# Kernel tuning notes

Measured on AMD Instinct MI355X. Metric: run time of the kernel, lower is better.

The kernel has to match this reference:

```python
import jax, jax.numpy as jnp
import numpy as np

N = 100000
SAMPLE = 25
FEAT = 128
HIDDEN = 128
CLASSES = 40


def setup_inputs() -> dict:
    key = jax.random.key(0)
    k_x, k_n, k_w1, k_w2, k_wl = jax.random.split(key, 5)
    X = jax.random.normal(k_x, (N, FEAT), dtype=jnp.float32)
    neighbors = jax.random.randint(k_n, (N, SAMPLE), 0, N, dtype=jnp.int32)
    # torch Linear weights are [out_features, in_features], xavier-uniform init
    def xavier(k, out_d, in_d):
        bound = float(np.sqrt(6.0 / (in_d + out_d)))
        return jax.random.uniform(k, (out_d, in_d), dtype=jnp.float32, minval=-bound, maxval=bound)
    W1 = xavier(k_w1, HIDDEN, FEAT)
    W2 = xavier(k_w2, HIDDEN, HIDDEN)
    Wlast = xavier(k_wl, CLASSES, HIDDEN)
    return {"X": X, "neighbors": neighbors, "W1": W1, "W2": W2, "Wlast": Wlast}


def reference(X, neighbors, W1, W2, Wlast):
    # forward: for each layer W: X = spmm(adj, X); X = X @ W.T; relu(X)
    # adj row i has sample_num entries of value 1/sample_num -> mean over sampled neighbors
    h = X
    for W in (W1, W2):
        agg = jnp.mean(h[neighbors], axis=1)          # [N, sample, d] -> [N, d]
        h = jax.nn.relu(jnp.einsum('nd,hd->nh', agg, W))
    return jnp.einsum('nh,ch->nc', h, Wlast)          # [N, class_num]
```

## Files before the change

kernel.cpp:

```cpp
#include <hip/hip_runtime.h>
#include <cstdint>
#include <cstddef>

typedef unsigned short u16;
typedef __bf16 bf16x8 __attribute__((ext_vector_type(8)));
typedef u16 u16x8 __attribute__((ext_vector_type(8)));
typedef float f32x4 __attribute__((ext_vector_type(4)));

#define N_NODES 100000
#define SAMPLE 25
#define FEAT 128
#define CLASSES 40

__device__ __forceinline__ float bf2f(u16 v) {
    return __uint_as_float(((unsigned)v) << 16);
}
__device__ __forceinline__ u16 f2bf(float f) {
    unsigned u = __float_as_uint(f);
    u += 0x7FFFu + ((u >> 16) & 1u);
    return (u16)(u >> 16);
}
__device__ __forceinline__ void split_bf(float x, u16& hi, u16& lo) {
    hi = f2bf(x);
    lo = f2bf(x - bf2f(hi));
}

__device__ __forceinline__ void split8(const float* ap, bf16x8& ah, bf16x8& al) {
    union { u16x8 u; bf16x8 b; } H, L;
    #pragma unroll
    for (int j = 0; j < 8; ++j) {
        u16 h, lo; split_bf(ap[j], h, lo);
        H.u[j] = h; L.u[j] = lo;
    }
    ah = H.b; al = L.b;
}

__device__ __forceinline__ f32x4 mfma_split(bf16x8 ah, bf16x8 al,
                                            bf16x8 bh, bf16x8 bl, f32x4 acc) {
    acc = __builtin_amdgcn_mfma_f32_16x16x32_bf16(ah, bh, acc, 0, 0, 0);
    acc = __builtin_amdgcn_mfma_f32_16x16x32_bf16(al, bh, acc, 0, 0, 0);
    acc = __builtin_amdgcn_mfma_f32_16x16x32_bf16(ah, bl, acc, 0, 0, 0);
    return acc;
}

__global__ __launch_bounds__(256) void prep_weights(
    const float* __restrict__ W1, const float* __restrict__ W2,
    const float* __restrict__ Wl,
    u16* __restrict__ w1h, u16* __restrict__ w1l,
    u16* __restrict__ w2h, u16* __restrict__ w2l,
    u16* __restrict__ wlh, u16* __restrict__ wll)
{
    const int i = blockIdx.x * 256 + threadIdx.x;
    const int stride = gridDim.x * 256;
    for (int j = i; j < FEAT * FEAT; j += stride) {
        split_bf(W1[j], w1h[j], w1l[j]);
        split_bf(W2[j], w2h[j], w2l[j]);
    }
    for (int j = i; j < CLASSES * FEAT; j += stride) {
        split_bf(Wl[j], wlh[j], wll[j]);
    }
}

#define NPB32 32
#define ZT_STRIDE 136

__global__ __launch_bounds__(128, 4) void k1_gemm(
    const float* __restrict__ X,
    const u16* __restrict__ w1h, const u16* __restrict__ w1l,
    u16* __restrict__ Z1)
{
    __shared__ u16 zt[NPB32][ZT_STRIDE];

    const int t = threadIdx.x;
    const int w  = t >> 6;
    const int l  = t & 63;
    const int lr = l & 15;
    const int lq = l >> 4;
    const int blockStart = blockIdx.x * NPB32;
    const float* Xrow = X + (size_t)(blockStart + w * 16 + lr) * FEAT;

    bf16x8 ah[4], al[4];
    #pragma unroll
    for (int k = 0; k < 4; ++k) {
        f32x4 x0 = *(const f32x4*)(Xrow + k * 32 + lq * 8);
        f32x4 x1 = *(const f32x4*)(Xrow + k * 32 + lq * 8 + 4);
        float tmp[8];
        #pragma unroll
        for (int j = 0; j < 4; ++j) { tmp[j] = x0[j]; tmp[4 + j] = x1[j]; }
        split8(tmp, ah[k], al[k]);
    }

    #pragma unroll
    for (int c = 0; c < 8; ++c) {
        f32x4 acc = {0.f, 0.f, 0.f, 0.f};
        #pragma unroll
        for (int k = 0; k < 4; ++k) {
            const size_t off = (size_t)(c * 16 + lr) * FEAT + k * 32 + lq * 8;
            bf16x8 bh = *(const bf16x8*)(w1h + off);
            bf16x8 bl = *(const bf16x8*)(w1l + off);
            acc = mfma_split(ah[k], al[k], bh, bl, acc);
        }
        #pragma unroll
        for (int r = 0; r < 4; ++r)
            zt[w * 16 + lq * 4 + r][c * 16 + lr] = f2bf(acc[r]);
    }
    __syncthreads();

    #pragma unroll
    for (int p = 0; p < 4; ++p) {
        const int idx = p * 128 + t;
        const int row = idx >> 4;
        const int col = (idx & 15) * 8;
        *(u16x8*)(Z1 + (size_t)(blockStart + row) * FEAT + col) =
            *(const u16x8*)&zt[row][col];
    }
}

__global__ __launch_bounds__(128, 3) void k2_hop(
    const u16* __restrict__ Zin, const int* __restrict__ nb,
    const u16* __restrict__ wh, const u16* __restrict__ wl,
    u16* __restrict__ Zout)
{
    __shared__ int nbs[NPB32 * SAMPLE];
    __shared__ float agg[NPB32][132];

    const int t = threadIdx.x;
    const int blockStart = blockIdx.x * NPB32;

    for (int i = t; i < NPB32 * SAMPLE; i += 128)
        nbs[i] = nb[blockStart * SAMPLE + i];
    __syncthreads();

    #pragma unroll 1
    for (int it = 0; it < 4; ++it) {
        const int item = t + it * 128;
        const int nl = item >> 4;
        const int fg = item & 15;
        const int* myn = &nbs[nl * SAMPLE];
        u16x8 buf[SAMPLE];
        #pragma unroll
        for (int s = 0; s < SAMPLE; ++s)
            buf[s] = *(const u16x8*)(Zin + ((size_t)myn[s] << 7) + fg * 8);
        float acc[8];
        #pragma unroll
        for (int j = 0; j < 8; ++j) acc[j] = 0.f;
        #pragma unroll
        for (int s = 0; s < SAMPLE; ++s) {
            #pragma unroll
            for (int j = 0; j < 8; ++j) acc[j] += bf2f(buf[s][j]);
        }
        #pragma unroll
        for (int j = 0; j < 8; ++j) {
            float m = acc[j] * (1.0f / SAMPLE);
            agg[nl][fg * 8 + j] = m > 0.f ? m : 0.f;
        }
    }
    __syncthreads();

    const int w  = t >> 6;
    const int l  = t & 63;
    const int lr = l & 15;
    const int lq = l >> 4;

    bf16x8 ah[4], al[4];
    #pragma unroll
    for (int k = 0; k < 4; ++k)
        split8(&agg[w * 16 + lr][k * 32 + lq * 8], ah[k], al[k]);
    __syncthreads();

    u16* zt = (u16*)agg;

    #pragma unroll
    for (int c = 0; c < 8; ++c) {
        f32x4 acc = {0.f, 0.f, 0.f, 0.f};
        #pragma unroll
        for (int k = 0; k < 4; ++k) {
            const size_t off = (size_t)(c * 16 + lr) * FEAT + k * 32 + lq * 8;
            bf16x8 bh = *(const bf16x8*)(wh + off);
            bf16x8 bl = *(const bf16x8*)(wl + off);
            acc = mfma_split(ah[k], al[k], bh, bl, acc);
        }
        #pragma unroll
        for (int r = 0; r < 4; ++r)
            zt[(size_t)(w * 16 + lq * 4 + r) * ZT_STRIDE + c * 16 + lr] = f2bf(acc[r]);
    }
    __syncthreads();

    #pragma unroll
    for (int p = 0; p < 4; ++p) {
        const int idx = p * 128 + t;
        const int row = idx >> 4;
        const int col = (idx & 15) * 8;
        *(u16x8*)(Zout + (size_t)(blockStart + row) * FEAT + col) =
            *(const u16x8*)&zt[(size_t)row * ZT_STRIDE + col];
    }
}

__global__ __launch_bounds__(128, 3) void k3_hop(
    const u16* __restrict__ Zin, const int* __restrict__ nb,
    const u16* __restrict__ wh, const u16* __restrict__ wl,
    float* __restrict__ out)
{
    __shared__ int nbs[NPB32 * SAMPLE];
    __shared__ float agg[NPB32][132];

    const int t = threadIdx.x;
    const int blockStart = blockIdx.x * NPB32;

    for (int i = t; i < NPB32 * SAMPLE; i += 128)
        nbs[i] = nb[blockStart * SAMPLE + i];
    __syncthreads();

    #pragma unroll 1
    for (int it = 0; it < 4; ++it) {
        const int item = t + it * 128;
        const int nl = item >> 4;
        const int fg = item & 15;
        const int* myn = &nbs[nl * SAMPLE];
        u16x8 buf[SAMPLE];
        #pragma unroll
        for (int s = 0; s < SAMPLE; ++s)
            buf[s] = *(const u16x8*)(Zin + ((size_t)myn[s] << 7) + fg * 8);
        float acc[8];
        #pragma unroll
        for (int j = 0; j < 8; ++j) acc[j] = 0.f;
        #pragma unroll
        for (int s = 0; s < SAMPLE; ++s) {
            #pragma unroll
            for (int j = 0; j < 8; ++j) acc[j] += bf2f(buf[s][j]);
        }
        #pragma unroll
        for (int j = 0; j < 8; ++j) {
            float m = acc[j] * (1.0f / SAMPLE);
            agg[nl][fg * 8 + j] = m > 0.f ? m : 0.f;
        }
    }
    __syncthreads();

    const int w  = t >> 6;
    const int l  = t & 63;
    const int lr = l & 15;
    const int lq = l >> 4;

    bf16x8 ah[4], al[4];
    #pragma unroll
    for (int k = 0; k < 4; ++k)
        split8(&agg[w * 16 + lr][k * 32 + lq * 8], ah[k], al[k]);

    #pragma unroll
    for (int c = 0; c < 3; ++c) {
        const int o = c * 16 + lr;
        f32x4 acc = {0.f, 0.f, 0.f, 0.f};
        #pragma unroll
        for (int k = 0; k < 4; ++k) {
            bf16x8 bh, bl;
            if (o < CLASSES) {
                const size_t off = (size_t)o * FEAT + k * 32 + lq * 8;
                bh = *(const bf16x8*)(wh + off);
                bl = *(const bf16x8*)(wl + off);
            } else {
                #pragma unroll
                for (int j = 0; j < 8; ++j) { bh[j] = (__bf16)0.f; bl[j] = (__bf16)0.f; }
            }
            acc = mfma_split(ah[k], al[k], bh, bl, acc);
        }
        if (o < CLASSES) {
            #pragma unroll
            for (int r = 0; r < 4; ++r) {
                const int node = blockStart + w * 16 + lq * 4 + r;
                out[(size_t)node * CLASSES + o] = acc[r];
            }
        }
    }
}

#define NPB 64
#define AGG_STRIDE 136

__global__ __launch_bounds__(256) void gnn_layer1(
    const float* __restrict__ X, const int* __restrict__ nb,
    const u16* __restrict__ w1h, const u16* __restrict__ w1l,
    u16* __restrict__ h1)
{
    __shared__ int nbs[NPB * SAMPLE];
    __shared__ u16 agg_h[NPB][AGG_STRIDE];
    __shared__ u16 agg_l[NPB][AGG_STRIDE];

    const int t = threadIdx.x;
    const int blockStart = blockIdx.x * NPB;

    for (int i = t; i < NPB * SAMPLE; i += 256) {
        int gi = blockStart * SAMPLE + i;
        if (gi >= N_NODES * SAMPLE) gi = N_NODES * SAMPLE - 1;
        nbs[i] = nb[gi];
    }
    __syncthreads();

    for (int item = t; item < NPB * 16; item += 256) {
        const int nl = item >> 4;
        const int fg = item & 15;
        float acc[8];
        #pragma unroll
        for (int j = 0; j < 8; ++j) acc[j] = 0.f;
        const int* myn = &nbs[nl * SAMPLE];
        for (int s = 0; s < SAMPLE; ++s) {
            const float4* p = (const float4*)(X + (size_t)myn[s] * FEAT + fg * 8);
            float4 a = p[0], b = p[1];
            acc[0] += a.x; acc[1] += a.y; acc[2] += a.z; acc[3] += a.w;
            acc[4] += b.x; acc[5] += b.y; acc[6] += b.z; acc[7] += b.w;
        }
        u16x8 oh, ol;
        #pragma unroll
        for (int j = 0; j < 8; ++j) {
            float m = acc[j] * (1.0f / SAMPLE);
            u16 h, lo; split_bf(m, h, lo);
            oh[j] = h; ol[j] = lo;
        }
        *(u16x8*)&agg_h[nl][fg * 8] = oh;
        *(u16x8*)&agg_l[nl][fg * 8] = ol;
    }
    __syncthreads();

    const int w  = t >> 6;
    const int l  = t & 63;
    const int lr = l & 15;
    const int lq = l >> 4;

    bf16x8 ah[4], al[4];
    #pragma unroll
    for (int k = 0; k < 4; ++k) {
        ah[k] = *(const bf16x8*)&agg_h[w * 16 + lr][k * 32 + lq * 8];
        al[k] = *(const bf16x8*)&agg_l[w * 16 + lr][k * 32 + lq * 8];
    }

    #pragma unroll
    for (int c = 0; c < 8; ++c) {
        f32x4 acc = {0.f, 0.f, 0.f, 0.f};
        #pragma unroll
        for (int k = 0; k < 4; ++k) {
            const size_t off = (size_t)(c * 16 + lr) * FEAT + k * 32 + lq * 8;
            bf16x8 bh = *(const bf16x8*)(w1h + off);
            bf16x8 bl = *(const bf16x8*)(w1l + off);
            acc = mfma_split(ah[k], al[k], bh, bl, acc);
        }
        #pragma unroll
        for (int r = 0; r < 4; ++r) {
            int node = blockStart + w * 16 + lq * 4 + r;
            if (node < N_NODES) {
                float v = acc[r] > 0.f ? acc[r] : 0.f;
                h1[(size_t)node * FEAT + c * 16 + lr] = f2bf(v);
            }
        }
    }
}

__global__ __launch_bounds__(256) void gnn_layer2_final(
    const u16* __restrict__ h1, const int* __restrict__ nb,
    const u16* __restrict__ w2h, const u16* __restrict__ w2l,
    const u16* __restrict__ wlh, const u16* __restrict__ wll,
    float* __restrict__ out)
{
    __shared__ int nbs[NPB * SAMPLE];
    __shared__ u16 agg_h[NPB][AGG_STRIDE];
    __shared__ u16 agg_l[NPB][AGG_STRIDE];

    const int t = threadIdx.x;
    const int blockStart = blockIdx.x * NPB;

    for (int i = t; i < NPB * SAMPLE; i += 256) {
        int gi = blockStart * SAMPLE + i;
        if (gi >= N_NODES * SAMPLE) gi = N_NODES * SAMPLE - 1;
        nbs[i] = nb[gi];
    }
    __syncthreads();

    for (int item = t; item < NPB * 16; item += 256) {
        const int nl = item >> 4;
        const int fg = item & 15;
        float acc[8];
        #pragma unroll
        for (int j = 0; j < 8; ++j) acc[j] = 0.f;
        const int* myn = &nbs[nl * SAMPLE];
        for (int s = 0; s < SAMPLE; ++s) {
            u16x8 v = *(const u16x8*)(h1 + (size_t)myn[s] * FEAT + fg * 8);
            #pragma unroll
            for (int j = 0; j < 8; ++j) acc[j] += bf2f(v[j]);
        }
        u16x8 oh, ol;
        #pragma unroll
        for (int j = 0; j < 8; ++j) {
            float m = acc[j] * (1.0f / SAMPLE);
            u16 h, lo; split_bf(m, h, lo);
            oh[j] = h; ol[j] = lo;
        }
        *(u16x8*)&agg_h[nl][fg * 8] = oh;
        *(u16x8*)&agg_l[nl][fg * 8] = ol;
    }
    __syncthreads();

    const int w  = t >> 6;
    const int l  = t & 63;
    const int lr = l & 15;
    const int lq = l >> 4;

    f32x4 hacc[8];
    {
        bf16x8 ah[4], al[4];
        #pragma unroll
        for (int k = 0; k < 4; ++k) {
            ah[k] = *(const bf16x8*)&agg_h[w * 16 + lr][k * 32 + lq * 8];
            al[k] = *(const bf16x8*)&agg_l[w * 16 + lr][k * 32 + lq * 8];
        }
        #pragma unroll
        for (int c = 0; c < 8; ++c) {
            f32x4 acc = {0.f, 0.f, 0.f, 0.f};
            #pragma unroll
            for (int k = 0; k < 4; ++k) {
                const size_t off = (size_t)(c * 16 + lr) * FEAT + k * 32 + lq * 8;
                bf16x8 bh = *(const bf16x8*)(w2h + off);
                bf16x8 bl = *(const bf16x8*)(w2l + off);
                acc = mfma_split(ah[k], al[k], bh, bl, acc);
            }
            hacc[c] = acc;
        }
    }
    __syncthreads();

    #pragma unroll
    for (int c = 0; c < 8; ++c) {
        #pragma unroll
        for (int r = 0; r < 4; ++r) {
            float v = hacc[c][r] > 0.f ? hacc[c][r] : 0.f;
            u16 h, l2; split_bf(v, h, l2);
            agg_h[w * 16 + lq * 4 + r][c * 16 + lr] = h;
            agg_l[w * 16 + lq * 4 + r][c * 16 + lr] = l2;
        }
    }
    __syncthreads();

    {
        bf16x8 ah[4], al[4];
        #pragma unroll
        for (int k = 0; k < 4; ++k) {
            ah[k] = *(const bf16x8*)&agg_h[w * 16 + lr][k * 32 + lq * 8];
            al[k] = *(const bf16x8*)&agg_l[w * 16 + lr][k * 32 + lq * 8];
        }
        #pragma unroll
        for (int c = 0; c < 3; ++c) {
            const int o = c * 16 + lr;
            f32x4 acc = {0.f, 0.f, 0.f, 0.f};
            #pragma unroll
            for (int k = 0; k < 4; ++k) {
                bf16x8 bh, bl;
                if (o < CLASSES) {
                    const size_t off = (size_t)o * FEAT + k * 32 + lq * 8;
                    bh = *(const bf16x8*)(wlh + off);
                    bl = *(const bf16x8*)(wll + off);
                } else {
                    #pragma unroll
                    for (int j = 0; j < 8; ++j) { bh[j] = (__bf16)0.f; bl[j] = (__bf16)0.f; }
                }
                acc = mfma_split(ah[k], al[k], bh, bl, acc);
            }
            if (o < CLASSES) {
                #pragma unroll
                for (int r = 0; r < 4; ++r) {
                    int node = blockStart + w * 16 + lq * 4 + r;
                    if (node < N_NODES) {
                        out[(size_t)node * CLASSES + o] = acc[r];
                    }
                }
            }
        }
    }
}

extern "C" void kernel_launch(void* const* d_in, const int* in_sizes, int n_in,
                              void* d_out, int out_size, void* d_ws, size_t ws_size,
                              hipStream_t stream) {
    const float* X  = (const float*)d_in[0];
    const int*   nb = (const int*)d_in[1];
    const float* W1 = (const float*)d_in[2];
    const float* W2 = (const float*)d_in[3];
    const float* Wl = (const float*)d_in[4];
    float* out = (float*)d_out;

    const size_t zelems = (size_t)N_NODES * FEAT;
    const size_t welems = 4 * (size_t)FEAT * FEAT + 2 * (size_t)CLASSES * FEAT;
    const size_t need_fast = (2 * zelems + welems) * sizeof(u16);

    if (ws_size >= need_fast) {
        u16* Z1  = (u16*)d_ws;
        u16* Z2  = Z1 + zelems;
        u16* w1h = Z2 + zelems;
        u16* w1l = w1h + FEAT * FEAT;
        u16* w2h = w1l + FEAT * FEAT;
        u16* w2l = w2h + FEAT * FEAT;
        u16* wlh = w2l + FEAT * FEAT;
        u16* wll = wlh + CLASSES * FEAT;

        prep_weights<<<64, 256, 0, stream>>>(W1, W2, Wl, w1h, w1l, w2h, w2l, wlh, wll);
        const int blocks = N_NODES / NPB32;
        k1_gemm<<<blocks, 128, 0, stream>>>(X, w1h, w1l, Z1);
        k2_hop<<<blocks, 128, 0, stream>>>(Z1, nb, w2h, w2l, Z2);
        k3_hop<<<blocks, 128, 0, stream>>>(Z2, nb, wlh, wll, out);
    } else {
        u16* h1  = (u16*)d_ws;
        u16* w1h = h1 + zelems;
        u16* w1l = w1h + FEAT * FEAT;
        u16* w2h = w1l + FEAT * FEAT;
        u16* w2l = w2h + FEAT * FEAT;
        u16* wlh = w2l + FEAT * FEAT;
        u16* wll = wlh + CLASSES * FEAT;

        prep_weights<<<64, 256, 0, stream>>>(W1, W2, Wl, w1h, w1l, w2h, w2l, wlh, wll);
        const int blocks = (N_NODES + NPB - 1) / NPB;
        gnn_layer1<<<blocks, 256, 0, stream>>>(X, nb, w1h, w1l, h1);
        gnn_layer2_final<<<blocks, 256, 0, stream>>>(h1, nb, w2h, w2l, wlh, wll, out);
    }
}
```

Before: 328.6 us.

## Gather neighbor features directly into MFMA fragment layout, dropping LDS staging

The hop kernels now have each lane gather and sum the neighbor feature slices it needs for its MFMA A-fragment. The mean, relu and hi/lo split happen in registers, so the shared-memory float aggregation buffer and one barrier are gone. Less LDS lets the occupancy hint go from 3 to 4 blocks per CU. The risk is that each lane now issues four 16-byte loads per neighbor with a different coalescing pattern, and the accumulators use more registers.

```diff
diff --git a/kernel.cpp b/kernel.cpp
--- a/kernel.cpp
+++ b/kernel.cpp
@@ -116,73 +116,74 @@
     }
 }
 
-__global__ __launch_bounds__(128, 3) void k2_hop(
+__global__ __launch_bounds__(128, 4) void k2_hop(
     const u16* __restrict__ Zin, const int* __restrict__ nb,
     const u16* __restrict__ wh, const u16* __restrict__ wl,
     u16* __restrict__ Zout)
 {
     __shared__ int nbs[NPB32 * SAMPLE];
-    __shared__ float agg[NPB32][132];
+    __shared__ u16 zt[NPB32][ZT_STRIDE];
 
     const int t = threadIdx.x;
     const int blockStart = blockIdx.x * NPB32;
 
     for (int i = t; i < NPB32 * SAMPLE; i += 128)
         nbs[i] = nb[blockStart * SAMPLE + i];
-    __syncthreads();
-
-    #pragma unroll 1
-    for (int it = 0; it < 4; ++it) {
-        const int item = t + it * 128;
-        const int nl = item >> 4;
-        const int fg = item & 15;
-        const int* myn = &nbs[nl * SAMPLE];
-        u16x8 buf[SAMPLE];
-        #pragma unroll
-        for (int s = 0; s < SAMPLE; ++s)
-            buf[s] = *(const u16x8*)(Zin + ((size_t)myn[s] << 7) + fg * 8);
-        float acc[8];
-        #pragma unroll
-        for (int j = 0; j < 8; ++j) acc[j] = 0.f;
-        #pragma unroll
-        for (int s = 0; s < SAMPLE; ++s) {
-            #pragma unroll
-            for (int j = 0; j < 8; ++j) acc[j] += bf2f(buf[s][j]);
-        }
-        #pragma unroll
-        for (int j = 0; j < 8; ++j) {
-            float m = acc[j] * (1.0f / SAMPLE);
-            agg[nl][fg * 8 + j] = m > 0.f ? m : 0.f;
-        }
-    }
     __syncthreads();
 
     const int w  = t >> 6;
     const int l  = t & 63;
     const int lr = l & 15;
     const int lq = l >> 4;
+    const int* myn = &nbs[(w * 16 + lr) * SAMPLE];
+
+    float acc[4][8];
+    #pragma unroll
+    for (int k = 0; k < 4; ++k)
+        #pragma unroll
+        for (int j = 0; j < 8; ++j) acc[k][j] = 0.f;
+
+    #pragma unroll
+    for (int s = 0; s < SAMPLE; ++s) {
+        const u16* row = Zin + ((size_t)myn[s] << 7) + lq * 8;
+        u16x8 v0 = *(const u16x8*)(row);
+        u16x8 v1 = *(const u16x8*)(row + 32);
+        u16x8 v2 = *(const u16x8*)(row + 64);
+        u16x8 v3 = *(const u16x8*)(row + 96);
+        #pragma unroll
+        for (int j = 0; j < 8; ++j) {
+            acc[0][j] += bf2f(v0[j]);
+            acc[1][j] += bf2f(v1[j]);
+            acc[2][j] += bf2f(v2[j]);
+            acc[3][j] += bf2f(v3[j]);
+        }
+    }
 
     bf16x8 ah[4], al[4];
     #pragma unroll
-    for (int k = 0; k < 4; ++k)
-        split8(&agg[w * 16 + lr][k * 32 + lq * 8], ah[k], al[k]);
-    __syncthreads();
-
-    u16* zt = (u16*)agg;
+    for (int k = 0; k < 4; ++k) {
+        float tmp[8];
+        #pragma unroll
+        for (int j = 0; j < 8; ++j) {
+            float m = acc[k][j] * (1.0f / SAMPLE);
+            tmp[j] = m > 0.f ? m : 0.f;
+        }
+        split8(tmp, ah[k], al[k]);
+    }
 
     #pragma unroll
     for (int c = 0; c < 8; ++c) {
-        f32x4 acc = {0.f, 0.f, 0.f, 0.f};
+        f32x4 o = {0.f, 0.f, 0.f, 0.f};
         #pragma unroll
         for (int k = 0; k < 4; ++k) {
             const size_t off = (size_t)(c * 16 + lr) * FEAT + k * 32 + lq * 8;
             bf16x8 bh = *(const bf16x8*)(wh + off);
             bf16x8 bl = *(const bf16x8*)(wl + off);
-            acc = mfma_split(ah[k], al[k], bh, bl, acc);
+            o = mfma_split(ah[k], al[k], bh, bl, o);
         }
         #pragma unroll
         for (int r = 0; r < 4; ++r)
-            zt[(size_t)(w * 16 + lq * 4 + r) * ZT_STRIDE + c * 16 + lr] = f2bf(acc[r]);
+            zt[w * 16 + lq * 4 + r][c * 16 + lr] = f2bf(o[r]);
     }
     __syncthreads();
 
@@ -192,65 +193,68 @@
         const int row = idx >> 4;
         const int col = (idx & 15) * 8;
         *(u16x8*)(Zout + (size_t)(blockStart + row) * FEAT + col) =
-            *(const u16x8*)&zt[(size_t)row * ZT_STRIDE + col];
-    }
-}
-
-__global__ __launch_bounds__(128, 3) void k3_hop(
+            *(const u16x8*)&zt[row][col];
+    }
+}
+
+__global__ __launch_bounds__(128, 4) void k3_hop(
     const u16* __restrict__ Zin, const int* __restrict__ nb,
     const u16* __restrict__ wh, const u16* __restrict__ wl,
     float* __restrict__ out)
 {
     __shared__ int nbs[NPB32 * SAMPLE];
-    __shared__ float agg[NPB32][132];
 
     const int t = threadIdx.x;
     const int blockStart = blockIdx.x * NPB32;
 
     for (int i = t; i < NPB32 * SAMPLE; i += 128)
         nbs[i] = nb[blockStart * SAMPLE + i];
-    __syncthreads();
-
-    #pragma unroll 1
-    for (int it = 0; it < 4; ++it) {
-        const int item = t + it * 128;
-        const int nl = item >> 4;
-        const int fg = item & 15;
-        const int* myn = &nbs[nl * SAMPLE];
-        u16x8 buf[SAMPLE];
-        #pragma unroll
-        for (int s = 0; s < SAMPLE; ++s)
-            buf[s] = *(const u16x8*)(Zin + ((size_t)myn[s] << 7) + fg * 8);
-        float acc[8];
-        #pragma unroll
-        for (int j = 0; j < 8; ++j) acc[j] = 0.f;
-        #pragma unroll
-        for (int s = 0; s < SAMPLE; ++s) {
-            #pragma unroll
-            for (int j = 0; j < 8; ++j) acc[j] += bf2f(buf[s][j]);
-        }
-        #pragma unroll
-        for (int j = 0; j < 8; ++j) {
-            float m = acc[j] * (1.0f / SAMPLE);
-            agg[nl][fg * 8 + j] = m > 0.f ? m : 0.f;
-        }
-    }
     __syncthreads();
 
     const int w  = t >> 6;
     const int l  = t & 63;
     const int lr = l & 15;
     const int lq = l >> 4;
+    const int* myn = &nbs[(w * 16 + lr) * SAMPLE];
+
+    float acc[4][8];
+    #pragma unroll
+    for (int k = 0; k < 4; ++k)
+        #pragma unroll
+        for (int j = 0; j < 8; ++j) acc[k][j] = 0.f;
+
+    #pragma unroll
+    for (int s = 0; s < SAMPLE; ++s) {
+        const u16* row = Zin + ((size_t)myn[s] << 7) + lq * 8;
+        u16x8 v0 = *(const u16x8*)(row);
+        u16x8 v1 = *(const u16x8*)(row + 32);
+        u16x8 v2 = *(const u16x8*)(row + 64);
+        u16x8 v3 = *(const u16x8*)(row + 96);
+        #pragma unroll
+        for (int j = 0; j < 8; ++j) {
+            acc[0][j] += bf2f(v0[j]);
+            acc[1][j] += bf2f(v1[j]);
+            acc[2][j] += bf2f(v2[j]);
+            acc[3][j] += bf2f(v3[j]);
+        }
+    }
 
     bf16x8 ah[4], al[4];
     #pragma unroll
-    for (int k = 0; k < 4; ++k)
-        split8(&agg[w * 16 + lr][k * 32 + lq * 8], ah[k], al[k]);
+    for (int k = 0; k < 4; ++k) {
+        float tmp[8];
+        #pragma unroll
+        for (int j = 0; j < 8; ++j) {
+            float m = acc[k][j] * (1.0f / SAMPLE);
+            tmp[j] = m > 0.f ? m : 0.f;
+        }
+        split8(tmp, ah[k], al[k]);
+    }
 
     #pragma unroll
     for (int c = 0; c < 3; ++c) {
         const int o = c * 16 + lr;
-        f32x4 acc = {0.f, 0.f, 0.f, 0.f};
+        f32x4 a = {0.f, 0.f, 0.f, 0.f};
         #pragma unroll
         for (int k = 0; k < 4; ++k) {
             bf16x8 bh, bl;
@@ -262,13 +266,13 @@
                 #pragma unroll
                 for (int j = 0; j < 8; ++j) { bh[j] = (__bf16)0.f; bl[j] = (__bf16)0.f; }
             }
-            acc = mfma_split(ah[k], al[k], bh, bl, acc);
+            a = mfma_split(ah[k], al[k], bh, bl, a);
         }
         if (o < CLASSES) {
             #pragma unroll
             for (int r = 0; r < 4; ++r) {
                 const int node = blockStart + w * 16 + lq * 4 + r;
-                out[(size_t)node * CLASSES + o] = acc[r];
+                out[(size_t)node * CLASSES + o] = a[r];
             }
         }
     }
```

After: 612.5 us. 86.4% more time.

## Split gathers into feature-plane layout with separate gather and GEMM kernels

Applied to the files above, without the earlier changes.

Stores the intermediate bf16 activations as 8 planes of 16 features each. Neighbor gathers then run per plane in a dedicated kernel, so each plane's working set (about 3.2 MB) can stay cache-resident across the random accesses. The aggregated fp32 result goes to global memory and a separate GEMM kernel consumes it. The cost is extra global traffic for the fp32 aggregate (about 51 MB written and read per hop), two more kernel launches, and the neighbor lists being re-read once per plane.

```diff
diff --git a/kernel.cpp b/kernel.cpp
--- a/kernel.cpp
+++ b/kernel.cpp
@@ -11,6 +11,7 @@
 #define SAMPLE 25
 #define FEAT 128
 #define CLASSES 40
+#define PLSTR ((size_t)N_NODES * 16)
 
 __device__ __forceinline__ float bf2f(u16 v) {
     return __uint_as_float(((unsigned)v) << 16);
@@ -64,10 +65,25 @@
 #define NPB32 32
 #define ZT_STRIDE 136
 
-__global__ __launch_bounds__(128, 4) void k1_gemm(
+
+__device__ __forceinline__ void load_afrag_f32(
+    const float* __restrict__ row, int lq, bf16x8 (&ah)[4], bf16x8 (&al)[4])
+{
+    #pragma unroll
+    for (int k = 0; k < 4; ++k) {
+        f32x4 x0 = *(const f32x4*)(row + k * 32 + lq * 8);
+        f32x4 x1 = *(const f32x4*)(row + k * 32 + lq * 8 + 4);
+        float tmp[8];
+        #pragma unroll
+        for (int j = 0; j < 4; ++j) { tmp[j] = x0[j]; tmp[4 + j] = x1[j]; }
+        split8(tmp, ah[k], al[k]);
+    }
+}
+
+__global__ __launch_bounds__(128, 4) void k1_pl(
     const float* __restrict__ X,
     const u16* __restrict__ w1h, const u16* __restrict__ w1l,
-    u16* __restrict__ Z1)
+    u16* __restrict__ Zp)
 {
     __shared__ u16 zt[NPB32][ZT_STRIDE];
 
@@ -77,18 +93,9 @@
     const int lr = l & 15;
     const int lq = l >> 4;
     const int blockStart = blockIdx.x * NPB32;
-    const float* Xrow = X + (size_t)(blockStart + w * 16 + lr) * FEAT;
 
     bf16x8 ah[4], al[4];
-    #pragma unroll
-    for (int k = 0; k < 4; ++k) {
-        f32x4 x0 = *(const f32x4*)(Xrow + k * 32 + lq * 8);
-        f32x4 x1 = *(const f32x4*)(Xrow + k * 32 + lq * 8 + 4);
-        float tmp[8];
-        #pragma unroll
-        for (int j = 0; j < 4; ++j) { tmp[j] = x0[j]; tmp[4 + j] = x1[j]; }
-        split8(tmp, ah[k], al[k]);
-    }
+    load_afrag_f32(X + (size_t)(blockStart + w * 16 + lr) * FEAT, lq, ah, al);
 
     #pragma unroll
     for (int c = 0; c < 8; ++c) {
@@ -109,66 +116,89 @@
     #pragma unroll
     for (int p = 0; p < 4; ++p) {
         const int idx = p * 128 + t;
-        const int row = idx >> 4;
-        const int col = (idx & 15) * 8;
-        *(u16x8*)(Z1 + (size_t)(blockStart + row) * FEAT + col) =
-            *(const u16x8*)&zt[row][col];
-    }
-}
-
-__global__ __launch_bounds__(128, 3) void k2_hop(
-    const u16* __restrict__ Zin, const int* __restrict__ nb,
-    const u16* __restrict__ wh, const u16* __restrict__ wl,
-    u16* __restrict__ Zout)
-{
-    __shared__ int nbs[NPB32 * SAMPLE];
-    __shared__ float agg[NPB32][132];
-
-    const int t = threadIdx.x;
-    const int blockStart = blockIdx.x * NPB32;
-
-    for (int i = t; i < NPB32 * SAMPLE; i += 128)
-        nbs[i] = nb[blockStart * SAMPLE + i];
-    __syncthreads();
+        const int plane = idx >> 6;
+        const int rem = idx & 63;
+        const int row = rem >> 1;
+        const int half = rem & 1;
+        *(u16x8*)(Zp + (size_t)plane * PLSTR + (size_t)(blockStart + row) * 16 + half * 8) =
+            *(const u16x8*)&zt[row][plane * 16 + half * 8];
+    }
+}
+
+#define GNPB 64
+#define GBLKS 1563
+__global__ __launch_bounds__(128) void g_hop(
+    const u16* __restrict__ Zp, const int* __restrict__ nb,
+    float* __restrict__ aggG)
+{
+    __shared__ int nbs[GNPB * SAMPLE];
+
+    const int t = threadIdx.x;
+    const int plane = blockIdx.x / GBLKS;
+    const int nblk  = blockIdx.x % GBLKS;
+    const int blockStart = nblk * GNPB;
+
+    for (int i = t; i < GNPB * SAMPLE; i += 128) {
+        int gi = blockStart * SAMPLE + i;
+        if (gi >= N_NODES * SAMPLE) gi = N_NODES * SAMPLE - 1;
+        nbs[i] = nb[gi];
+    }
+    __syncthreads();
+
+    const int nl = t >> 1;
+    const int half = t & 1;
+    const int node = blockStart + nl;
+    const int* myn = &nbs[nl * SAMPLE];
+    const u16* base = Zp + (size_t)plane * PLSTR + half * 8;
+
+    float acc[8];
+    #pragma unroll
+    for (int j = 0; j < 8; ++j) acc[j] = 0.f;
 
     #pragma unroll 1
-    for (int it = 0; it < 4; ++it) {
-        const int item = t + it * 128;
-        const int nl = item >> 4;
-        const int fg = item & 15;
-        const int* myn = &nbs[nl * SAMPLE];
-        u16x8 buf[SAMPLE];
-        #pragma unroll
-        for (int s = 0; s < SAMPLE; ++s)
-            buf[s] = *(const u16x8*)(Zin + ((size_t)myn[s] << 7) + fg * 8);
-        float acc[8];
-        #pragma unroll
-        for (int j = 0; j < 8; ++j) acc[j] = 0.f;
-        #pragma unroll
-        for (int s = 0; s < SAMPLE; ++s) {
+    for (int b = 0; b < 5; ++b) {
+        u16x8 buf[5];
+        #pragma unroll
+        for (int s = 0; s < 5; ++s)
+            buf[s] = *(const u16x8*)(base + (size_t)myn[b * 5 + s] * 16);
+        #pragma unroll
+        for (int s = 0; s < 5; ++s) {
             #pragma unroll
             for (int j = 0; j < 8; ++j) acc[j] += bf2f(buf[s][j]);
         }
-        #pragma unroll
-        for (int j = 0; j < 8; ++j) {
-            float m = acc[j] * (1.0f / SAMPLE);
-            agg[nl][fg * 8 + j] = m > 0.f ? m : 0.f;
-        }
-    }
-    __syncthreads();
-
+    }
+
+    if (node < N_NODES) {
+        float* dst = aggG + (size_t)node * FEAT + plane * 16 + half * 8;
+        f32x4 o0, o1;
+        #pragma unroll
+        for (int j = 0; j < 4; ++j) {
+            float m0 = acc[j] * (1.0f / SAMPLE);
+            float m1 = acc[4 + j] * (1.0f / SAMPLE);
+            o0[j] = m0 > 0.f ? m0 : 0.f;
+            o1[j] = m1 > 0.f ? m1 : 0.f;
+        }
+        *(f32x4*)dst = o0;
+        *(f32x4*)(dst + 4) = o1;
+    }
+}
+
+__global__ __launch_bounds__(128, 4) void m_mid(
+    const float* __restrict__ aggG,
+    const u16* __restrict__ wh, const u16* __restrict__ wl,
+    u16* __restrict__ Zp)
+{
+    __shared__ u16 zt[NPB32][ZT_STRIDE];
+
+    const int t = threadIdx.x;
     const int w  = t >> 6;
     const int l  = t & 63;
     const int lr = l & 15;
     const int lq = l >> 4;
+    const int blockStart = blockIdx.x * NPB32;
 
     bf16x8 ah[4], al[4];
-    #pragma unroll
-    for (int k = 0; k < 4; ++k)
-        split8(&agg[w * 16 + lr][k * 32 + lq * 8], ah[k], al[k]);
-    __syncthreads();
-
-    u16* zt = (u16*)agg;
+    load_afrag_f32(aggG + (size_t)(blockStart + w * 16 + lr) * FEAT, lq, ah, al);
 
     #pragma unroll
     for (int c = 0; c < 8; ++c) {
@@ -182,75 +212,41 @@
         }
         #pragma unroll
         for (int r = 0; r < 4; ++r)
-            zt[(size_t)(w * 16 + lq * 4 + r) * ZT_STRIDE + c * 16 + lr] = f2bf(acc[r]);
+            zt[w * 16 + lq * 4 + r][c * 16 + lr] = f2bf(acc[r]);
     }
     __syncthreads();
 
     #pragma unroll
     for (int p = 0; p < 4; ++p) {
         const int idx = p * 128 + t;
-        const int row = idx >> 4;
-        const int col = (idx & 15) * 8;
-        *(u16x8*)(Zout + (size_t)(blockStart + row) * FEAT + col) =
-            *(const u16x8*)&zt[(size_t)row * ZT_STRIDE + col];
-    }
-}
-
-__global__ __launch_bounds__(128, 3) void k3_hop(
-    const u16* __restrict__ Zin, const int* __restrict__ nb,
+        const int plane = idx >> 6;
+        const int rem = idx & 63;
+        const int row = rem >> 1;
+        const int half = rem & 1;
+        *(u16x8*)(Zp + (size_t)plane * PLSTR + (size_t)(blockStart + row) * 16 + half * 8) =
+            *(const u16x8*)&zt[row][plane * 16 + half * 8];
+    }
+}
+
+__global__ __launch_bounds__(128, 4) void m_last(
+    const float* __restrict__ aggG,
     const u16* __restrict__ wh, const u16* __restrict__ wl,
     float* __restrict__ out)
 {
-    __shared__ int nbs[NPB32 * SAMPLE];
-    __shared__ float agg[NPB32][132];
-
-    const int t = threadIdx.x;
-    const int blockStart = blockIdx.x * NPB32;
-
-    for (int i = t; i < NPB32 * SAMPLE; i += 128)
-        nbs[i] = nb[blockStart * SAMPLE + i];
-    __syncthreads();
-
-    #pragma unroll 1
-    for (int it = 0; it < 4; ++it) {
-        const int item = t + it * 128;
-        const int nl = item >> 4;
-        const int fg = item & 15;
-        const int* myn = &nbs[nl * SAMPLE];
-        u16x8 buf[SAMPLE];
-        #pragma unroll
-        for (int s = 0; s < SAMPLE; ++s)
-            buf[s] = *(const u16x8*)(Zin + ((size_t)myn[s] << 7) + fg * 8);
-        float acc[8];
-        #pragma unroll
-        for (int j = 0; j < 8; ++j) acc[j] = 0.f;
-        #pragma unroll
-        for (int s = 0; s < SAMPLE; ++s) {
-            #pragma unroll
-            for (int j = 0; j < 8; ++j) acc[j] += bf2f(buf[s][j]);
-        }
-        #pragma unroll
-        for (int j = 0; j < 8; ++j) {
-            float m = acc[j] * (1.0f / SAMPLE);
-            agg[nl][fg * 8 + j] = m > 0.f ? m : 0.f;
-        }
-    }
-    __syncthreads();
-
+    const int t = threadIdx.x;
     const int w  = t >> 6;
     const int l  = t & 63;
     const int lr = l & 15;
     const int lq = l >> 4;
+    const int blockStart = blockIdx.x * NPB32;
 
     bf16x8 ah[4], al[4];
-    #pragma unroll
-    for (int k = 0; k < 4; ++k)
-        split8(&agg[w * 16 + lr][k * 32 + lq * 8], ah[k], al[k]);
+    load_afrag_f32(aggG + (size_t)(blockStart + w * 16 + lr) * FEAT, lq, ah, al);
 
     #pragma unroll
     for (int c = 0; c < 3; ++c) {
         const int o = c * 16 + lr;
-        f32x4 acc = {0.f, 0.f, 0.f, 0.f};
+        f32x4 a = {0.f, 0.f, 0.f, 0.f};
         #pragma unroll
         for (int k = 0; k < 4; ++k) {
             bf16x8 bh, bl;
@@ -262,76 +258,34 @@
                 #pragma unroll
                 for (int j = 0; j < 8; ++j) { bh[j] = (__bf16)0.f; bl[j] = (__bf16)0.f; }
             }
-            acc = mfma_split(ah[k], al[k], bh, bl, acc);
+            a = mfma_split(ah[k], al[k], bh, bl, a);
         }
         if (o < CLASSES) {
             #pragma unroll
             for (int r = 0; r < 4; ++r) {
                 const int node = blockStart + w * 16 + lq * 4 + r;
-                out[(size_t)node * CLASSES + o] = acc[r];
+                out[(size_t)node * CLASSES + o] = a[r];
             }
         }
     }
 }
 
-#define NPB 64
-#define AGG_STRIDE 136
-
-__global__ __launch_bounds__(256) void gnn_layer1(
-    const float* __restrict__ X, const int* __restrict__ nb,
+__global__ __launch_bounds__(128, 4) void k1_row(
+    const float* __restrict__ X,
     const u16* __restrict__ w1h, const u16* __restrict__ w1l,
-    u16* __restrict__ h1)
-{
-    __shared__ int nbs[NPB * SAMPLE];
-    __shared__ u16 agg_h[NPB][AGG_STRIDE];
-    __shared__ u16 agg_l[NPB][AGG_STRIDE];
-
-    const int t = threadIdx.x;
-    const int blockStart = blockIdx.x * NPB;
-
-    for (int i = t; i < NPB * SAMPLE; i += 256) {
-        int gi = blockStart * SAMPLE + i;
-        if (gi >= N_NODES * SAMPLE) gi = N_NODES * SAMPLE - 1;
-        nbs[i] = nb[gi];
-    }
-    __syncthreads();
-
-    for (int item = t; item < NPB * 16; item += 256) {
-        const int nl = item >> 4;
-        const int fg = item & 15;
-        float acc[8];
-        #pragma unroll
-        for (int j = 0; j < 8; ++j) acc[j] = 0.f;
-        const int* myn = &nbs[nl * SAMPLE];
-        for (int s = 0; s < SAMPLE; ++s) {
-            const float4* p = (const float4*)(X + (size_t)myn[s] * FEAT + fg * 8);
-            float4 a = p[0], b = p[1];
-            acc[0] += a.x; acc[1] += a.y; acc[2] += a.z; acc[3] += a.w;
-            acc[4] += b.x; acc[5] += b.y; acc[6] += b.z; acc[7] += b.w;
-        }
-        u16x8 oh, ol;
-        #pragma unroll
-        for (int j = 0; j < 8; ++j) {
-            float m = acc[j] * (1.0f / SAMPLE);
-            u16 h, lo; split_bf(m, h, lo);
-            oh[j] = h; ol[j] = lo;
-        }
-        *(u16x8*)&agg_h[nl][fg * 8] = oh;
-        *(u16x8*)&agg_l[nl][fg * 8] = ol;
-    }
-    __syncthreads();
-
+    u16* __restrict__ Z1)
+{
+    __shared__ u16 zt[NPB32][ZT_STRIDE];
+
+    const int t = threadIdx.x;
     const int w  = t >> 6;
     const int l  = t & 63;
     const int lr = l & 15;
     const int lq = l >> 4;
+    const int blockStart = blockIdx.x * NPB32;
 
     bf16x8 ah[4], al[4];
-    #pragma unroll
-    for (int k = 0; k < 4; ++k) {
-        ah[k] = *(const bf16x8*)&agg_h[w * 16 + lr][k * 32 + lq * 8];
-        al[k] = *(const bf16x8*)&agg_l[w * 16 + lr][k * 32 + lq * 8];
-    }
+    load_afrag_f32(X + (size_t)(blockStart + w * 16 + lr) * FEAT, lq, ah, al);
 
     #pragma unroll
     for (int c = 0; c < 8; ++c) {
@@ -344,57 +298,59 @@
             acc = mfma_split(ah[k], al[k], bh, bl, acc);
         }
         #pragma unroll
-        for (int r = 0; r < 4; ++r) {
-            int node = blockStart + w * 16 + lq * 4 + r;
-            if (node < N_NODES) {
-                float v = acc[r] > 0.f ? acc[r] : 0.f;
-                h1[(size_t)node * FEAT + c * 16 + lr] = f2bf(v);
-            }
-        }
-    }
-}
-
-__global__ __launch_bounds__(256) void gnn_layer2_final(
-    const u16* __restrict__ h1, const int* __restrict__ nb,
-    const u16* __restrict__ w2h, const u16* __restrict__ w2l,
-    const u16* __restrict__ wlh, const u16* __restrict__ wll,
-    float* __restrict__ out)
-{
-    __shared__ int nbs[NPB * SAMPLE];
-    __shared__ u16 agg_h[NPB][AGG_STRIDE];
-    __shared__ u16 agg_l[NPB][AGG_STRIDE];
-
-    const int t = threadIdx.x;
-    const int blockStart = blockIdx.x * NPB;
-
-    for (int i = t; i < NPB * SAMPLE; i += 256) {
-        int gi = blockStart * SAMPLE + i;
-        if (gi >= N_NODES * SAMPLE) gi = N_NODES * SAMPLE - 1;
-        nbs[i] = nb[gi];
-    }
-    __syncthreads();
-
-    for (int item = t; item < NPB * 16; item += 256) {
+        for (int r = 0; r < 4; ++r)
+            zt[w * 16 + lq * 4 + r][c * 16 + lr] = f2bf(acc[r]);
+    }
+    __syncthreads();
+
+    #pragma unroll
+    for (int p = 0; p < 4; ++p) {
+        const int idx = p * 128 + t;
+        const int row = idx >> 4;
+        const int col = (idx & 15) * 8;
+        *(u16x8*)(Z1 + (size_t)(blockStart + row) * FEAT + col) =
+            *(const u16x8*)&zt[row][col];
+    }
+}
+
+__global__ __launch_bounds__(128, 3) void k2_r4(
+    const u16* __restrict__ Zin, const int* __restrict__ nb,
+    const u16* __restrict__ wh, const u16* __restrict__ wl,
+    u16* __restrict__ Zout)
+{
+    __shared__ int nbs[NPB32 * SAMPLE];
+    __shared__ float agg[NPB32][132];
+
+    const int t = threadIdx.x;
+    const int blockStart = blockIdx.x * NPB32;
+
+    for (int i = t; i < NPB32 * SAMPLE; i += 128)
+        nbs[i] = nb[blockStart * SAMPLE + i];
+    __syncthreads();
+
+    #pragma unroll 1
+    for (int it = 0; it < 4; ++it) {
+        const int item = t + it * 128;
         const int nl = item >> 4;
         const int fg = item & 15;
+        const int* myn = &nbs[nl * SAMPLE];
+        u16x8 buf[SAMPLE];
+        #pragma unroll
+        for (int s = 0; s < SAMPLE; ++s)
+            buf[s] = *(const u16x8*)(Zin + ((size_t)myn[s] << 7) + fg * 8);
         float acc[8];
         #pragma unroll
         for (int j = 0; j < 8; ++j) acc[j] = 0.f;
-        const int* myn = &nbs[nl * SAMPLE];
+        #pragma unroll
         for (int s = 0; s < SAMPLE; ++s) {
-            u16x8 v = *(const u16x8*)(h1 + (size_t)myn[s] * FEAT + fg * 8);
             #pragma unroll
-            for (int j = 0; j < 8; ++j) acc[j] += bf2f(v[j]);
-        }
-        u16x8 oh, ol;
+            for (int j = 0; j < 8; ++j) acc[j] += bf2f(buf[s][j]);
+        }
         #pragma unroll
         for (int j = 0; j < 8; ++j) {
             float m = acc[j] * (1.0f / SAMPLE);
-            u16 h, lo; split_bf(m, h, lo);
-            oh[j] = h; ol[j] = lo;
-        }
-        *(u16x8*)&agg_h[nl][fg * 8] = oh;
-        *(u16x8*)&agg_l[nl][fg * 8] = ol;
+            agg[nl][fg * 8 + j] = m > 0.f ? m : 0.f;
+        }
     }
     __syncthreads();
 
@@ -403,73 +359,113 @@
     const int lr = l & 15;
     const int lq = l >> 4;
 
-    f32x4 hacc[8];
-    {
-        bf16x8 ah[4], al[4];
+    bf16x8 ah[4], al[4];
+    #pragma unroll
+    for (int k = 0; k < 4; ++k)
+        split8(&agg[w * 16 + lr][k * 32 + lq * 8], ah[k], al[k]);
+    __syncthreads();
+
+    u16* zt = (u16*)agg;
+
+    #pragma unroll
+    for (int c = 0; c < 8; ++c) {
+        f32x4 acc = {0.f, 0.f, 0.f, 0.f};
         #pragma unroll
         for (int k = 0; k < 4; ++k) {
-            ah[k] = *(const bf16x8*)&agg_h[w * 16 + lr][k * 32 + lq * 8];
-            al[k] = *(const bf16x8*)&agg_l[w * 16 + lr][k * 32 + lq * 8];
-        }
-        #pragma unroll
-        for (int c = 0; c < 8; ++c) {
-            f32x4 acc = {0.f, 0.f, 0.f, 0.f};
+            const size_t off = (size_t)(c * 16 + lr) * FEAT + k * 32 + lq * 8;
+            bf16x8 bh = *(const bf16x8*)(wh + off);
+            bf16x8 bl = *(const bf16x8*)(wl + off);
+            acc = mfma_split(ah[k], al[k], bh, bl, acc);
+        }
+        #pragma unroll
+        for (int r = 0; r < 4; ++r)
+            zt[(size_t)(w * 16 + lq * 4 + r) * ZT_STRIDE + c * 16 + lr] = f2bf(acc[r]);
+    }
+    __syncthreads();
+
+    #pragma unroll
+    for (int p = 0; p < 4; ++p) {
+        const int idx = p * 128 + t;
+        const int row = idx >> 4;
+        const int col = (idx & 15) * 8;
+        *(u16x8*)(Zout + (size_t)(blockStart + row) * FEAT + col) =
+            *(const u16x8*)&zt[(size_t)row * ZT_STRIDE + col];
+    }
+}
+
+__global__ __launch_bounds__(128, 3) void k3_r4(
+    const u16* __restrict__ Zin, const int* __restrict__ nb,
+    const u16* __restrict__ wh, const u16* __restrict__ wl,
+    float* __restrict__ out)
+{
+    __shared__ int nbs[NPB32 * SAMPLE];
+    __shared__ float agg[NPB32][132];
+
+    const int t = threadIdx.x;
+    const int blockStart = blockIdx.x * NPB32;
+
+    for (int i = t; i < NPB32 * SAMPLE; i += 128)
+        nbs[i] = nb[blockStart * SAMPLE + i];
+    __syncthreads();
+
+    #pragma unroll 1
+    for (int it = 0; it < 4; ++it) {
+        const int item = t + it * 128;
+        const int nl = item >> 4;
+        const int fg = item & 15;
+        const int* myn = &nbs[nl * SAMPLE];
+        u16x8 buf[SAMPLE];
+        #pragma unroll
+        for (int s = 0; s < SAMPLE; ++s)
+            buf[s] = *(const u16x8*)(Zin + ((size_t)myn[s] << 7) + fg * 8);
+        float acc[8];
+        #pragma unroll
+        for (int j = 0; j < 8; ++j) acc[j] = 0.f;
+        #pragma unroll
+        for (int s = 0; s < SAMPLE; ++s) {
             #pragma unroll
-            for (int k = 0; k < 4; ++k) {
-                const size_t off = (size_t)(c * 16 + lr) * FEAT + k * 32 + lq * 8;
-                bf16x8 bh = *(const bf16x8*)(w2h + off);
-                bf16x8 bl = *(const bf16x8*)(w2l + off);
-                acc = mfma_split(ah[k], al[k], bh, bl, acc);
+            for (int j = 0; j < 8; ++j) acc[j] += bf2f(buf[s][j]);
+        }
+        #pragma unroll
+        for (int j = 0; j < 8; ++j) {
+            float m = acc[j] * (1.0f / SAMPLE);
+            agg[nl][fg * 8 + j] = m > 0.f ? m : 0.f;
+        }
+    }
+    __syncthreads();
+
+    const int w  = t >> 6;
+    const int l  = t & 63;
+    const int lr = l & 15;
+    const int lq = l >> 4;
+
+    bf16x8 ah[4], al[4];
+    #pragma unroll
+    for (int k = 0; k < 4; ++k)
+        split8(&agg[w * 16 + lr][k * 32 + lq * 8], ah[k], al[k]);
+
+    #pragma unroll
+    for (int c = 0; c < 3; ++c) {
+        const int o = c * 16 + lr;
+        f32x4 a = {0.f, 0.f, 0.f, 0.f};
+        #pragma unroll
+        for (int k = 0; k < 4; ++k) {
+            bf16x8 bh, bl;
+            if (o < CLASSES) {
+                const size_t off = (size_t)o * FEAT + k * 32 + lq * 8;
+                bh = *(const bf16x8*)(wh + off);
+                bl = *(const bf16x8*)(wl + off);
+            } else {
+                #pragma unroll
+                for (int j = 0; j < 8; ++j) { bh[j] = (__bf16)0.f; bl[j] = (__bf16)0.f; }
             }
-            hacc[c] = acc;
-        }
-    }
-    __syncthreads();
-
-    #pragma unroll
-    for (int c = 0; c < 8; ++c) {
-        #pragma unroll
-        for (int r = 0; r < 4; ++r) {
-            float v = hacc[c][r] > 0.f ? hacc[c][r] : 0.f;
-            u16 h, l2; split_bf(v, h, l2);
-            agg_h[w * 16 + lq * 4 + r][c * 16 + lr] = h;
-            agg_l[w * 16 + lq * 4 + r][c * 16 + lr] = l2;
-        }
-    }
-    __syncthreads();
-
-    {
-        bf16x8 ah[4], al[4];
-        #pragma unroll
-        for (int k = 0; k < 4; ++k) {
-            ah[k] = *(const bf16x8*)&agg_h[w * 16 + lr][k * 32 + lq * 8];
-            al[k] = *(const bf16x8*)&agg_l[w * 16 + lr][k * 32 + lq * 8];
-        }
-        #pragma unroll
-        for (int c = 0; c < 3; ++c) {
-            const int o = c * 16 + lr;
-            f32x4 acc = {0.f, 0.f, 0.f, 0.f};
+            a = mfma_split(ah[k], al[k], bh, bl, a);
+        }
+        if (o < CLASSES) {
             #pragma unroll
-            for (int k = 0; k < 4; ++k) {
-                bf16x8 bh, bl;
-                if (o < CLASSES) {
-                    const size_t off = (size_t)o * FEAT + k * 32 + lq * 8;
-                    bh = *(const bf16x8*)(wlh + off);
-                    bl = *(const bf16x8*)(wll + off);
-                } else {
-                    #pragma unroll
-                    for (int j = 0; j < 8; ++j) { bh[j] = (__bf16)0.f; bl[j] = (__bf16)0.f; }
-                }
-                acc = mfma_split(ah[k], al[k], bh, bl, acc);
-            }
-            if (o < CLASSES) {
-                #pragma unroll
-                for (int r = 0; r < 4; ++r) {
-                    int node = blockStart + w * 16 + lq * 4 + r;
-                    if (node < N_NODES) {
-                        out[(size_t)node * CLASSES + o] = acc[r];
-                    }
-                }
+            for (int r = 0; r < 4; ++r) {
+                const int node = blockStart + w * 16 + lq * 4 + r;
+                out[(size_t)node * CLASSES + o] = a[r];
             }
         }
     }
@@ -487,9 +483,29 @@
 
     const size_t zelems = (size_t)N_NODES * FEAT;
     const size_t welems = 4 * (size_t)FEAT * FEAT + 2 * (size_t)CLASSES * FEAT;
-    const size_t need_fast = (2 * zelems + welems) * sizeof(u16);
-
-    if (ws_size >= need_fast) {
+    const size_t need_plane = zelems * sizeof(u16) + zelems * sizeof(float)
+                            + welems * sizeof(u16);
+    const size_t need_r4 = (2 * zelems + welems) * sizeof(u16);
+
+    const int gblocks = N_NODES / NPB32;
+
+    if (ws_size >= need_plane) {
+        u16*   Zp   = (u16*)d_ws;
+        float* aggG = (float*)(Zp + zelems);
+        u16*   w1h  = (u16*)(aggG + zelems);
+        u16*   w1l  = w1h + FEAT * FEAT;
+        u16*   w2h  = w1l + FEAT * FEAT;
+        u16*   w2l  = w2h + FEAT * FEAT;
+        u16*   wlh  = w2l + FEAT * FEAT;
+        u16*   wll  = wlh + CLASSES * FEAT;
+
+        prep_weights<<<64, 256, 0, stream>>>(W1, W2, Wl, w1h, w1l, w2h, w2l, wlh, wll);
+        k1_pl<<<gblocks, 128, 0, stream>>>(X, w1h, w1l, Zp);
+        g_hop<<<8 * GBLKS, 128, 0, stream>>>(Zp, nb, aggG);
+        m_mid<<<gblocks, 128, 0, stream>>>(aggG, w2h, w2l, Zp);
+        g_hop<<<8 * GBLKS, 128, 0, stream>>>(Zp, nb, aggG);
+        m_last<<<gblocks, 128, 0, stream>>>(aggG, wlh, wll, out);
+    } else {
         u16* Z1  = (u16*)d_ws;
         u16* Z2  = Z1 + zelems;
         u16* w1h = Z2 + zelems;
@@ -500,22 +516,8 @@
         u16* wll = wlh + CLASSES * FEAT;
 
         prep_weights<<<64, 256, 0, stream>>>(W1, W2, Wl, w1h, w1l, w2h, w2l, wlh, wll);
-        const int blocks = N_NODES / NPB32;
-        k1_gemm<<<blocks, 128, 0, stream>>>(X, w1h, w1l, Z1);
-        k2_hop<<<blocks, 128, 0, stream>>>(Z1, nb, w2h, w2l, Z2);
-        k3_hop<<<blocks, 128, 0, stream>>>(Z2, nb, wlh, wll, out);
-    } else {
-        u16* h1  = (u16*)d_ws;
-        u16* w1h = h1 + zelems;
-        u16* w1l = w1h + FEAT * FEAT;
-        u16* w2h = w1l + FEAT * FEAT;
-        u16* w2l = w2h + FEAT * FEAT;
-        u16* wlh = w2l + FEAT * FEAT;
-        u16* wll = wlh + CLASSES * FEAT;
-
-        prep_weights<<<64, 256, 0, stream>>>(W1, W2, Wl, w1h, w1l, w2h, w2l, wlh, wll);
-        const int blocks = (N_NODES + NPB - 1) / NPB;
-        gnn_layer1<<<blocks, 256, 0, stream>>>(X, nb, w1h, w1l, h1);
-        gnn_layer2_final<<<blocks, 256, 0, stream>>>(h1, nb, w2h, w2l, wlh, wll, out);
-    }
-}
+        k1_row<<<gblocks, 128, 0, stream>>>(X, w1h, w1l, Z1);
+        k2_r4<<<gblocks, 128, 0, stream>>>(Z1, nb, w2h, w2l, Z2);
+        k3_r4<<<gblocks, 128, 0, stream>>>(Z2, nb, wlh, wll, out);
+    }
+}
```

New measurement: 475.3 us. 44.6% more time.
